# Kernel optimization log

Measured on AMD Instinct MI355X. Metric: run time of the kernel, lower is better.

The kernel has to match this reference:

```python
import jax, jax.numpy as jnp
import numpy as np

B, S, DIN, DOUT = 8, 2048, 4096, 4096
THRESH = 0.1
LN_EPS = 1e-5

def setup_inputs() -> dict:
    key = jax.random.key(0)
    k_x, k_w = jax.random.split(key)
    x = jax.random.normal(k_x, (B, S, DIN), dtype=jnp.float32)
    # BitNet-style init: uniform(-0.1, 0.1)
    weight = (jax.random.uniform(k_w, (DOUT, DIN), dtype=jnp.float32) - 0.5) * 0.2
    bias = jnp.zeros((DOUT,), dtype=jnp.float32)
    scale = jnp.ones((DOUT,), dtype=jnp.float32)
    ln_gamma = jnp.ones((DOUT,), dtype=jnp.float32)
    ln_beta = jnp.zeros((DOUT,), dtype=jnp.float32)
    quant_scale = jnp.ones((1,), dtype=jnp.float32) * 10.0  # init per module
    return {"x": x, "weight": weight, "bias": bias, "scale": scale,
            "ln_gamma": ln_gamma, "ln_beta": ln_beta, "quant_scale": quant_scale}

def reference(x, weight, bias, scale, ln_gamma, ln_beta, quant_scale):
    # Ternary weight: sign(w), zeroed where |w| < threshold
    tern_w = jnp.where(jnp.abs(weight) < THRESH, 0.0, jnp.sign(weight))  # [DOUT, DIN]
    # Linear (F.linear computes x @ W^T + b) then learned per-channel scale
    y = jnp.einsum('bsd,od->bso', x, tern_w) + bias
    y = y * scale
    # LayerNorm over last dim (affine)
    mu = jnp.mean(y, axis=-1, keepdims=True)
    var = jnp.mean(jnp.square(y - mu), axis=-1, keepdims=True)
    y = (y - mu) * jax.lax.rsqrt(var + LN_EPS) * ln_gamma + ln_beta
    # tanh + round quantization to 8-bit grid
    y = jnp.tanh(y / quant_scale)
    y = jnp.round(y * 127.0) / 127.0
    return y
```

## Files before the change

kernel.cpp:

```cpp
#include <hip/hip_runtime.h>
#include <math.h>

#define B_   8
#define S_   2048
#define DIN_ 4096
#define DOUT_ 4096
#define THRESH_ 0.1f
#define LN_EPS_ 1e-5f

#define NROWS (B_ * S_)

__global__ __launch_bounds__(256) void lbe_scan_kernel(
    const float* __restrict__ w, int* __restrict__ cnt,
    int* __restrict__ list, int cap) {
  int idx = blockIdx.x * blockDim.x + threadIdx.x;
  const int total4 = (DOUT_ * DIN_) / 4;
  if (idx >= total4) return;
  float4 v = reinterpret_cast<const float4*>(w)[idx];
  const float* vp = &v.x;
#pragma unroll
  for (int j = 0; j < 4; ++j) {
    float wv = vp[j];
    if (fabsf(wv) >= THRESH_) {
      int flat = idx * 4 + j;
      int e = (flat << 1) | (wv < 0.f ? 1 : 0);
      int pos = atomicAdd(cnt, 1);
      if (pos < cap) list[pos] = e;
    }
  }
}

__global__ __launch_bounds__(256) void lbe_row_kernel(
    const float* __restrict__ x, const float* __restrict__ bias,
    const float* __restrict__ scale, const float* __restrict__ gamma,
    const float* __restrict__ beta, const float* __restrict__ qs,
    const int* __restrict__ cnt, const int* __restrict__ list, int cap,
    float* __restrict__ out) {
  __shared__ float sdot[DOUT_];
  __shared__ float sred[16];
  __shared__ float sstats[2];

  const int tid = threadIdx.x;
  const int row = blockIdx.x;
  const float* __restrict__ xr = x + (size_t)row * DIN_;

#pragma unroll
  for (int k = 0; k < DOUT_ / 256; ++k) sdot[tid + k * 256] = 0.f;
  __syncthreads();

  int n = *cnt;
  if (n > cap) n = cap;
  for (int e = tid; e < n; e += 256) {
    int ev = list[e];
    int flat = ev >> 1;
    int o = flat >> 12;
    int i = flat & (DIN_ - 1);
    float c = xr[i];
    if (ev & 1) c = -c;
    atomicAdd(&sdot[o], c);
  }
  __syncthreads();

  float s1 = 0.f, s2 = 0.f;
  float yv[DOUT_ / 256];
#pragma unroll
  for (int k = 0; k < DOUT_ / 256; ++k) {
    int o = tid + k * 256;
    float y = (sdot[o] + bias[o]) * scale[o];
    yv[k] = y;
    s1 += y;
    s2 += y * y;
  }

#pragma unroll
  for (int off = 32; off > 0; off >>= 1) {
    s1 += __shfl_down(s1, off);
    s2 += __shfl_down(s2, off);
  }
  int wid = tid >> 6, lane = tid & 63;
  if (lane == 0) { sred[wid] = s1; sred[8 + wid] = s2; }
  __syncthreads();
  if (tid == 0) {
    float a = 0.f, b = 0.f;
#pragma unroll
    for (int wv = 0; wv < 4; ++wv) { a += sred[wv]; b += sred[8 + wv]; }
    float mu = a * (1.f / DOUT_);
    float var = b * (1.f / DOUT_) - mu * mu;
    if (var < 0.f) var = 0.f;
    sstats[0] = mu;
    sstats[1] = rsqrtf(var + LN_EPS_);
  }
  __syncthreads();
  const float mu = sstats[0];
  const float rs = sstats[1];
  const float iq = 1.f / qs[0];

  float* __restrict__ orow = out + (size_t)row * DOUT_;
#pragma unroll
  for (int k = 0; k < DOUT_ / 256; ++k) {
    int o = tid + k * 256;
    float yn = (yv[k] - mu) * rs * gamma[o] + beta[o];
    float t = tanhf(yn * iq);
    orow[o] = rintf(t * 127.f) * (1.f / 127.f);
  }
}

extern "C" void kernel_launch(void* const* d_in, const int* in_sizes, int n_in,
                              void* d_out, int out_size, void* d_ws, size_t ws_size,
                              hipStream_t stream) {
  const float* x     = (const float*)d_in[0];
  const float* w     = (const float*)d_in[1];
  const float* bias  = (const float*)d_in[2];
  const float* scale = (const float*)d_in[3];
  const float* gamma = (const float*)d_in[4];
  const float* beta  = (const float*)d_in[5];
  const float* qs    = (const float*)d_in[6];
  float* out = (float*)d_out;

  int* cnt = (int*)d_ws;
  int* list = (int*)((char*)d_ws + 256);
  long long avail = (long long)ws_size - 256;
  int cap = avail > 0 ? (int)(avail / 4) : 0;
  if (cap > (1 << 24)) cap = 1 << 24;

  hipMemsetAsync(d_ws, 0, 4, stream);

  {
    const int total4 = (DOUT_ * DIN_) / 4;
    int blocks = (total4 + 255) / 256;
    lbe_scan_kernel<<<blocks, 256, 0, stream>>>(w, cnt, list, cap);
  }
  lbe_row_kernel<<<NROWS, 256, 0, stream>>>(x, bias, scale, gamma, beta, qs,
                                            cnt, list, cap, out);
}
```

Before: 465.4 us.

## Split LayerNorm stats into separate kernels and batch rows with vectorized fast-tanh output

Mean and variance are now computed from a bias*scale baseline plus per-row corrections for the sparse ternary entries, in separate base and stats kernels. The row kernel no longer needs a shared-memory accumulator with atomics or a block reduction. It handles 8 rows per block, keeps the per-channel parameters in registers, uses float4 stores and replaces tanhf with an exp/rcp approximation. Both the stats correction (quadratic in the number of nonzeros) and the per-thread compare-accumulate over the whole nonzero list only stay cheap when very few weights pass the threshold. Dense weights would make it far slower.

```diff
diff --git a/kernel.cpp b/kernel.cpp
--- a/kernel.cpp
+++ b/kernel.cpp
@@ -9,6 +9,15 @@
 #define LN_EPS_ 1e-5f
 
 #define NROWS (B_ * S_)
+#define RPB 8
+
+__device__ __forceinline__ float qtanh(float z, float iq) {
+  float t = z * iq;
+  t = fminf(fmaxf(t, -9.f), 9.f);
+  float e2 = __expf(2.f * t);
+  float r = (e2 - 1.f) * __builtin_amdgcn_rcpf(e2 + 1.f);
+  return rintf(r * 127.f) * (1.f / 127.f);
+}
 
 __global__ __launch_bounds__(256) void lbe_scan_kernel(
     const float* __restrict__ w, int* __restrict__ cnt,
@@ -30,78 +39,132 @@
   }
 }
 
+__global__ __launch_bounds__(256) void lbe_base_kernel(
+    const float* __restrict__ bias, const float* __restrict__ scale,
+    float* __restrict__ sq) {
+  int tid = threadIdx.x;
+  float s = 0.f, q = 0.f;
+#pragma unroll
+  for (int k = 0; k < 4; ++k) {
+    float4 b  = reinterpret_cast<const float4*>(bias)[tid + k * 256];
+    float4 sc = reinterpret_cast<const float4*>(scale)[tid + k * 256];
+    float p;
+    p = b.x * sc.x; s += p; q = fmaf(p, p, q);
+    p = b.y * sc.y; s += p; q = fmaf(p, p, q);
+    p = b.z * sc.z; s += p; q = fmaf(p, p, q);
+    p = b.w * sc.w; s += p; q = fmaf(p, p, q);
+  }
+#pragma unroll
+  for (int off = 32; off > 0; off >>= 1) {
+    s += __shfl_xor(s, off);
+    q += __shfl_xor(q, off);
+  }
+  __shared__ float red[8];
+  int wid = tid >> 6, lane = tid & 63;
+  if (lane == 0) { red[wid] = s; red[4 + wid] = q; }
+  __syncthreads();
+  if (tid == 0) {
+    sq[0] = red[0] + red[1] + red[2] + red[3];
+    sq[1] = red[4] + red[5] + red[6] + red[7];
+  }
+}
+
+__global__ __launch_bounds__(256) void lbe_stats_kernel(
+    const float* __restrict__ x, const float* __restrict__ bias,
+    const float* __restrict__ scale, const int* __restrict__ cnt,
+    const int* __restrict__ list, int cap, const float* __restrict__ sq,
+    float* __restrict__ murs) {
+  int row = blockIdx.x * blockDim.x + threadIdx.x;
+  if (row >= NROWS) return;
+  int n = *cnt; if (n > cap) n = cap;
+  const float* __restrict__ xr = x + (size_t)row * DIN_;
+  float dS = 0.f, dQ = 0.f;
+  for (int e = 0; e < n; ++e) {
+    int ev = list[e];
+    int o = ev >> 13;
+    bool first = true;
+    for (int e2 = 0; e2 < e; ++e2)
+      if ((list[e2] >> 13) == o) { first = false; break; }
+    if (!first) continue;
+    int i = (ev >> 1) & (DIN_ - 1);
+    float dotO = (ev & 1) ? -xr[i] : xr[i];
+    for (int e2 = e + 1; e2 < n; ++e2) {
+      int ev2 = list[e2];
+      if ((ev2 >> 13) == o) {
+        float c2 = xr[(ev2 >> 1) & (DIN_ - 1)];
+        dotO += (ev2 & 1) ? -c2 : c2;
+      }
+    }
+    float bo = bias[o], so = scale[o];
+    float t1 = (dotO + bo) * so;
+    float t0 = bo * so;
+    dS += dotO * so;
+    dQ += t1 * t1 - t0 * t0;
+  }
+  float S = sq[0] + dS, Q = sq[1] + dQ;
+  float mu = S * (1.f / DOUT_);
+  float var = Q * (1.f / DOUT_) - mu * mu;
+  if (var < 0.f) var = 0.f;
+  murs[row] = mu;
+  murs[NROWS + row] = rsqrtf(var + LN_EPS_);
+}
+
 __global__ __launch_bounds__(256) void lbe_row_kernel(
     const float* __restrict__ x, const float* __restrict__ bias,
     const float* __restrict__ scale, const float* __restrict__ gamma,
     const float* __restrict__ beta, const float* __restrict__ qs,
     const int* __restrict__ cnt, const int* __restrict__ list, int cap,
-    float* __restrict__ out) {
-  __shared__ float sdot[DOUT_];
-  __shared__ float sred[16];
-  __shared__ float sstats[2];
-
+    const float* __restrict__ murs, float* __restrict__ out) {
   const int tid = threadIdx.x;
-  const int row = blockIdx.x;
-  const float* __restrict__ xr = x + (size_t)row * DIN_;
-
-#pragma unroll
-  for (int k = 0; k < DOUT_ / 256; ++k) sdot[tid + k * 256] = 0.f;
-  __syncthreads();
-
-  int n = *cnt;
-  if (n > cap) n = cap;
-  for (int e = tid; e < n; e += 256) {
-    int ev = list[e];
-    int flat = ev >> 1;
-    int o = flat >> 12;
-    int i = flat & (DIN_ - 1);
-    float c = xr[i];
-    if (ev & 1) c = -c;
-    atomicAdd(&sdot[o], c);
-  }
-  __syncthreads();
-
-  float s1 = 0.f, s2 = 0.f;
-  float yv[DOUT_ / 256];
-#pragma unroll
-  for (int k = 0; k < DOUT_ / 256; ++k) {
-    int o = tid + k * 256;
-    float y = (sdot[o] + bias[o]) * scale[o];
-    yv[k] = y;
-    s1 += y;
-    s2 += y * y;
-  }
-
-#pragma unroll
-  for (int off = 32; off > 0; off >>= 1) {
-    s1 += __shfl_down(s1, off);
-    s2 += __shfl_down(s2, off);
-  }
-  int wid = tid >> 6, lane = tid & 63;
-  if (lane == 0) { sred[wid] = s1; sred[8 + wid] = s2; }
-  __syncthreads();
-  if (tid == 0) {
-    float a = 0.f, b = 0.f;
-#pragma unroll
-    for (int wv = 0; wv < 4; ++wv) { a += sred[wv]; b += sred[8 + wv]; }
-    float mu = a * (1.f / DOUT_);
-    float var = b * (1.f / DOUT_) - mu * mu;
-    if (var < 0.f) var = 0.f;
-    sstats[0] = mu;
-    sstats[1] = rsqrtf(var + LN_EPS_);
-  }
-  __syncthreads();
-  const float mu = sstats[0];
-  const float rs = sstats[1];
-  const float iq = 1.f / qs[0];
-
-  float* __restrict__ orow = out + (size_t)row * DOUT_;
-#pragma unroll
-  for (int k = 0; k < DOUT_ / 256; ++k) {
-    int o = tid + k * 256;
-    float yn = (yv[k] - mu) * rs * gamma[o] + beta[o];
-    float t = tanhf(yn * iq);
-    orow[o] = rintf(t * 127.f) * (1.f / 127.f);
+  float4 b4[4], s4[4], g4[4], e4[4];
+#pragma unroll
+  for (int k = 0; k < 4; ++k) {
+    int o4 = tid + k * 256;
+    b4[k] = reinterpret_cast<const float4*>(bias)[o4];
+    s4[k] = reinterpret_cast<const float4*>(scale)[o4];
+    g4[k] = reinterpret_cast<const float4*>(gamma)[o4];
+    e4[k] = reinterpret_cast<const float4*>(beta)[o4];
+  }
+  int n = *cnt; if (n > cap) n = cap;
+  const float iq = __builtin_amdgcn_rcpf(qs[0]);
+
+  const int row0 = blockIdx.x * RPB;
+  for (int r = 0; r < RPB; ++r) {
+    const int row = row0 + r;
+    const float* __restrict__ xr = x + (size_t)row * DIN_;
+    float4 d[4];
+#pragma unroll
+    for (int k = 0; k < 4; ++k) d[k] = make_float4(0.f, 0.f, 0.f, 0.f);
+    for (int e = 0; e < n; ++e) {
+      int ev = list[e];
+      int o = ev >> 13;
+      float c = xr[(ev >> 1) & (DIN_ - 1)];
+      if (ev & 1) c = -c;
+#pragma unroll
+      for (int k = 0; k < 4; ++k) {
+        int base = (tid + k * 256) << 2;
+        d[k].x += (o == base + 0) ? c : 0.f;
+        d[k].y += (o == base + 1) ? c : 0.f;
+        d[k].z += (o == base + 2) ? c : 0.f;
+        d[k].w += (o == base + 3) ? c : 0.f;
+      }
+    }
+    const float mu = murs[row];
+    const float rs = murs[NROWS + row];
+    float* __restrict__ orow = out + (size_t)row * DOUT_;
+#pragma unroll
+    for (int k = 0; k < 4; ++k) {
+      float4 y, rr;
+      y.x = (d[k].x + b4[k].x) * s4[k].x;
+      y.y = (d[k].y + b4[k].y) * s4[k].y;
+      y.z = (d[k].z + b4[k].z) * s4[k].z;
+      y.w = (d[k].w + b4[k].w) * s4[k].w;
+      rr.x = qtanh(fmaf((y.x - mu) * rs, g4[k].x, e4[k].x), iq);
+      rr.y = qtanh(fmaf((y.y - mu) * rs, g4[k].y, e4[k].y), iq);
+      rr.z = qtanh(fmaf((y.z - mu) * rs, g4[k].z, e4[k].z), iq);
+      rr.w = qtanh(fmaf((y.w - mu) * rs, g4[k].w, e4[k].w), iq);
+      reinterpret_cast<float4*>(orow)[tid + k * 256] = rr;
+    }
   }
 }
 
@@ -117,9 +180,12 @@
   const float* qs    = (const float*)d_in[6];
   float* out = (float*)d_out;
 
-  int* cnt = (int*)d_ws;
-  int* list = (int*)((char*)d_ws + 256);
-  long long avail = (long long)ws_size - 256;
+  int*   cnt  = (int*)d_ws;
+  float* sq   = (float*)((char*)d_ws + 16);
+  float* murs = (float*)((char*)d_ws + 256);
+  const size_t list_off = 256 + (size_t)2 * NROWS * 4;
+  int* list = (int*)((char*)d_ws + list_off);
+  long long avail = (long long)ws_size - (long long)list_off;
   int cap = avail > 0 ? (int)(avail / 4) : 0;
   if (cap > (1 << 24)) cap = 1 << 24;
 
@@ -127,9 +193,11 @@
 
   {
     const int total4 = (DOUT_ * DIN_) / 4;
-    int blocks = (total4 + 255) / 256;
-    lbe_scan_kernel<<<blocks, 256, 0, stream>>>(w, cnt, list, cap);
-  }
-  lbe_row_kernel<<<NROWS, 256, 0, stream>>>(x, bias, scale, gamma, beta, qs,
-                                            cnt, list, cap, out);
-}
+    lbe_scan_kernel<<<(total4 + 255) / 256, 256, 0, stream>>>(w, cnt, list, cap);
+  }
+  lbe_base_kernel<<<1, 256, 0, stream>>>(bias, scale, sq);
+  lbe_stats_kernel<<<NROWS / 256, 256, 0, stream>>>(x, bias, scale, cnt, list,
+                                                    cap, sq, murs);
+  lbe_row_kernel<<<NROWS / RPB, 256, 0, stream>>>(x, bias, scale, gamma, beta,
+                                                  qs, cnt, list, cap, murs, out);
+}
```

Result: faster. 442.6 us (-4.9%).
